# Performance work log

Measured on AMD Instinct MI355X. Metric: run time of the kernel, lower is better.

The kernel has to match this reference:

```python
import jax, jax.numpy as jnp
import numpy as np
from math import factorial as _fact

# ---- sizes / hyperparams (match init_kwargs) ----
N_NODES, N_EDGES = 8192, 131072
C, H, NRAD, NUM_LAYERS = 64, 64, 8, 2
R_MAX, AVG_NN = 5.0, 16.0
LS = (0, 1, 2)  # irreps degrees carried by node features and edge SH

# ---- real-basis Clebsch-Gordan coefficients (computed once in numpy) ----
def _cg_scalar(j1, m1, j2, m2, j3, m3):
    if m1 + m2 != m3:
        return 0.0
    pre = ((2*j3+1) * _fact(j1+j2-j3) * _fact(j1-j2+j3) * _fact(-j1+j2+j3)
           / _fact(j1+j2+j3+1)) ** 0.5
    pre *= (_fact(j1+m1)*_fact(j1-m1)*_fact(j2+m2)*_fact(j2-m2)
            * _fact(j3+m3)*_fact(j3-m3)) ** 0.5
    s = 0.0
    for k in range(max(0, j2-j3-m1, j1+m2-j3), min(j1+j2-j3, j1-m1, j2+m2)+1):
        s += (-1)**k / (_fact(k)*_fact(j1+j2-j3-k)*_fact(j1-m1-k)
                        * _fact(j2+m2-k)*_fact(j3-j2+m1+k)*_fact(j3-j1-m2+k))
    return pre * s

def _U_real(l):
    # unitary: Y_real = U @ Y_complex, components ordered m=-l..l
    U = np.zeros((2*l+1, 2*l+1), dtype=complex)
    s2 = 2 ** -0.5
    for m in range(-l, l+1):
        if m > 0:
            U[m+l, m+l] = (-1)**m * s2
            U[m+l, -m+l] = s2
        elif m == 0:
            U[l, l] = 1.0
        else:
            U[m+l, m+l] = 1j*s2
            U[m+l, -m+l] = -1j*(-1)**(-m)*s2
    return U

def _real_cg(l1, l2, l3):
    Cc = np.zeros((2*l1+1, 2*l2+1, 2*l3+1))
    for i1, m1 in enumerate(range(-l1, l1+1)):
        for i2, m2 in enumerate(range(-l2, l2+1)):
            m3 = m1 + m2
            if abs(m3) <= l3:
                Cc[i1, i2, m3+l3] = _cg_scalar(l1, m1, l2, m2, l3, m3)
    U1, U2, U3 = _U_real(l1), _U_real(l2), _U_real(l3)
    W = np.einsum('ia,jb,kc,abc->ijk', U1.conj(), U2.conj(), U3, Cc.astype(complex))
    W = W.real if np.linalg.norm(W.real) >= np.linalg.norm(W.imag) else W.imag
    W = W / np.linalg.norm(W) * (2*l3+1) ** 0.5  # component-style normalization
    return jnp.asarray(W, dtype=jnp.float32)

PATHS = [(l1, l2, l3) for l1 in LS for l2 in LS for l3 in LS
         if abs(l1 - l2) <= l3 <= l1 + l2]  # 15 tensor-product paths
CGS = [_real_cg(*p) for p in PATHS]
N_PATHS = len(PATHS)


def _sph(u):
    # real spherical harmonics of unit vectors, l=0,1,2, m=-l..l ordering
    x, y, z = u[:, 0], u[:, 1], u[:, 2]
    sh0 = jnp.ones((u.shape[0], 1), u.dtype)
    sh1 = jnp.sqrt(3.0) * jnp.stack([y, z, x], axis=-1)
    sh2 = jnp.stack([jnp.sqrt(15.0)*x*y, jnp.sqrt(15.0)*y*z,
                     jnp.sqrt(5.0)/2*(3*z*z - 1.0),
                     jnp.sqrt(15.0)*x*z, jnp.sqrt(15.0)/2*(x*x - y*y)], axis=-1)
    return (sh0, sh1, sh2)


def _forward(positions, embed, w_proj, mlp_w1, mlp_b1, mlp_w2, mlp_b2, mlp_w3,
             lin_self, gate_w, gate_b, species, senders, receivers):
    n = positions.shape[0]
    rel = (positions[receivers] - positions[senders]) / R_MAX  # [E,3]
    d = jnp.linalg.norm(rel, axis=-1)                          # [E]
    u = rel / jnp.maximum(d, 1e-6)[:, None]
    sh = _sph(u)
    freqs = jnp.arange(1, NRAD + 1, dtype=positions.dtype)
    xr = jnp.clip(d, 1e-4, 1.0)[:, None]
    basis = jnp.sqrt(2.0) * jnp.sin(freqs * jnp.pi * xr) / xr  # Bessel [E,NRAD]
    cut = 0.5 * (jnp.cos(jnp.pi * jnp.clip(d, 0.0, 1.0)) + 1.0)  # smooth cutoff

    # initial species embedding -> scalar (0e) features; l>0 start at zero
    x0 = embed[species] @ w_proj                                # [N,C]
    feats = [x0[:, :, None],
             jnp.zeros((n, C, 3), x0.dtype),
             jnp.zeros((n, C, 5), x0.dtype)]

    inv_sqrt_nn = 1.0 / jnp.sqrt(jnp.asarray(AVG_NN, x0.dtype))
    for i in range(NUM_LAYERS):
        # radial MLP -> per-path, per-channel edge weights
        h = jax.nn.silu(basis @ mlp_w1[i] + mlp_b1[i])
        h = jax.nn.silu(h @ mlp_w2[i] + mlp_b2[i])
        w = (h @ mlp_w3[i]).reshape(-1, N_PATHS, C) * cut[:, None, None]
        xg = [feats[l][senders] for l in LS]                    # edge gather
        msgs = [0.0, 0.0, 0.0]
        for p, (l1, l2, l3) in enumerate(PATHS):
            m = jnp.einsum('eci,ej,ijk->eck', xg[l1], sh[l2], CGS[p])
            msgs[l3] = msgs[l3] + m * w[:, p, :, None]
        agg = [jax.ops.segment_sum(msgs[l], receivers, num_segments=n) * inv_sqrt_nn
               for l in LS]
        # self-interaction linears + gated nonlinearity + skip
        y = [jnp.einsum('ncm,cd->ndm', agg[l], lin_self[i, l]) for l in LS]
        feats[0] = feats[0] + jax.nn.silu(y[0])
        g_in = feats[0][:, :, 0]                                # [N,C] scalars
        for l in (1, 2):
            g = jax.nn.sigmoid(g_in @ gate_w[i, l-1] + gate_b[i, l-1])
            feats[l] = feats[l] + g[:, :, None] * y[l]

    # alpha = 0.5 ** l per irrep, then flatten to [N, C*(1+3+5)]
    return jnp.concatenate([(feats[l] * (0.5 ** l)).reshape(n, -1) for l in LS],
                           axis=-1)


def setup_inputs() -> dict:
    key = jax.random.key(0)
    ks = jax.random.split(key, 12)
    f32 = jnp.float32
    return {
        'positions': jax.random.normal(ks[0], (N_NODES, 3), f32),
        'species': jax.random.randint(ks[1], (N_NODES,), 0, 5),
        'senders': jax.random.randint(ks[2], (N_EDGES,), 0, N_NODES),
        'receivers': jax.random.randint(ks[3], (N_EDGES,), 0, N_NODES),
        'embed': jax.random.normal(ks[4], (5, 32), f32),
        'w_proj': jax.random.normal(ks[5], (32, C), f32) / jnp.sqrt(32.0),
        'mlp_w1': jax.random.normal(ks[6], (NUM_LAYERS, NRAD, H), f32) / jnp.sqrt(float(NRAD)),
        'mlp_b1': jnp.zeros((NUM_LAYERS, H), f32),
        'mlp_w2': jax.random.normal(ks[7], (NUM_LAYERS, H, H), f32) / jnp.sqrt(float(H)),
        'mlp_b2': jnp.zeros((NUM_LAYERS, H), f32),
        'mlp_w3': jax.random.normal(ks[8], (NUM_LAYERS, H, N_PATHS * C), f32) / jnp.sqrt(float(H)),
        'lin_self': jax.random.normal(ks[9], (NUM_LAYERS, 3, C, C), f32) / jnp.sqrt(float(C)),
        'gate_w': jax.random.normal(ks[10], (NUM_LAYERS, 2, C, C), f32) / jnp.sqrt(float(C)),
        'gate_b': jnp.zeros((NUM_LAYERS, 2, C), f32),
    }


def reference(positions, species, senders, receivers, embed, w_proj, mlp_w1,
              mlp_b1, mlp_w2, mlp_b2, mlp_w3, lin_self, gate_w, gate_b):
    return _forward(positions, embed, w_proj, mlp_w1, mlp_b1, mlp_w2, mlp_b2,
                    mlp_w3, lin_self, gate_w, gate_b, species, senders, receivers)
```

## Files before the change

### kernel.cpp

```cpp
#include <hip/hip_runtime.h>
#include <cmath>
#include <algorithm>

#define N_NODES 8192
#define N_EDGES 131072
#define NPATHS 15
#define FPN 576
#define NODE_BLK 8
#define SWROW 968

typedef unsigned short ushortx;
typedef unsigned int uintx;
typedef short short8 __attribute__((ext_vector_type(8)));
typedef float f32x4 __attribute__((ext_vector_type(4)));

constexpr int PL1[NPATHS] = {0,0,0,1,1,1,1,1,1,2,2,2,2,2,2};
constexpr int PL2[NPATHS] = {0,1,2,0,1,1,1,2,2,0,1,1,2,2,2};
constexpr int PL3[NPATHS] = {0,1,2,1,0,1,2,1,2,2,1,2,0,1,2};
constexpr int CGOFF[NPATHS] = {0,1,10,35,44,53,80,125,170,245,270,315,390,415,490};
constexpr int CGTOT = 615;
constexpr int BOFF[3] = {0,1,4};

struct CGTable { float v[CGTOT]; };

constexpr double cfact(int n){ double r=1.0; for (int i=2;i<=n;++i) r*=i; return r; }
constexpr double csqrt(double x){
  if (x <= 0.0) return 0.0;
  double g = x < 1.0 ? 1.0 : x, p = 0.0;
  while (g != p){ p = g; g = 0.5*(g + x/g); }
  return g;
}
constexpr int cmax2(int a,int b){ return a>b?a:b; }
constexpr int cmin2(int a,int b){ return a<b?a:b; }

constexpr double cg_scalar_c(int j1,int m1,int j2,int m2,int j3,int m3){
  if (m1+m2 != m3) return 0.0;
  double pre = csqrt((2.0*j3+1.0)*cfact(j1+j2-j3)*cfact(j1-j2+j3)*cfact(-j1+j2+j3)/cfact(j1+j2+j3+1));
  pre *= csqrt(cfact(j1+m1)*cfact(j1-m1)*cfact(j2+m2)*cfact(j2-m2)*cfact(j3+m3)*cfact(j3-m3));
  double s = 0.0;
  int kmin = cmax2(0, cmax2(j2-j3-m1, j1+m2-j3));
  int kmax = cmin2(j1+j2-j3, cmin2(j1-m1, j2+m2));
  for (int k=kmin;k<=kmax;++k){
    double t = 1.0/(cfact(k)*cfact(j1+j2-j3-k)*cfact(j1-m1-k)*cfact(j2+m2-k)*cfact(j3-j2+m1+k)*cfact(j3-j1-m2+k));
    s += (k&1) ? -t : t;
  }
  return pre*s;
}

struct C2c { double re, im; };
constexpr C2c Uelem(int l, int a, int b){
  const double s2 = csqrt(0.5);
  const int m = a - l;
  C2c z{0.0, 0.0};
  if (m > 0){
    if (b ==  m+l) z = {((m&1)?-1.0:1.0)*s2, 0.0};
    else if (b == -m+l) z = {s2, 0.0};
  } else if (m == 0){
    if (b == l) z = {1.0, 0.0};
  } else {
    if (b ==  m+l) z = {0.0, s2};
    else if (b == -m+l) z = {0.0, -((((-m)&1))?-1.0:1.0)*s2};
  }
  return z;
}

constexpr CGTable build_cg(){
  CGTable t{};
  for (int p=0;p<NPATHS;++p){
    const int l1=PL1[p], l2=PL2[p], l3=PL3[p];
    const int n1=2*l1+1, n2=2*l2+1, n3=2*l3+1;
    double Cc[5][5][5] = {};
    for (int i1=0;i1<n1;++i1) for (int i2=0;i2<n2;++i2){
      int m1=i1-l1, m2=i2-l2, m3=m1+m2;
      if (m3 >= -l3 && m3 <= l3) Cc[i1][i2][m3+l3] = cg_scalar_c(l1,m1,l2,m2,l3,m3);
    }
    double Wre[5][5][5]={}, Wim[5][5][5]={};
    for (int i=0;i<n1;++i) for (int j=0;j<n2;++j) for (int k=0;k<n3;++k){
      double are=0.0, aim=0.0;
      for (int a=0;a<n1;++a) for (int b=0;b<n2;++b){
        int m3 = (a-l1)+(b-l2);
        if (m3 < -l3 || m3 > l3) continue;
        double cv = Cc[a][b][m3+l3];
        if (cv == 0.0) continue;
        C2c u1 = Uelem(l1,i,a);  u1.im = -u1.im;
        C2c u2 = Uelem(l2,j,b);  u2.im = -u2.im;
        C2c u3 = Uelem(l3,k,m3+l3);
        C2c u12{u1.re*u2.re - u1.im*u2.im, u1.re*u2.im + u1.im*u2.re};
        C2c tt {u12.re*u3.re - u12.im*u3.im, u12.re*u3.im + u12.im*u3.re};
        are += tt.re*cv; aim += tt.im*cv;
      }
      Wre[i][j][k]=are; Wim[i][j][k]=aim;
    }
    double nr=0.0, ni=0.0;
    for (int i=0;i<n1;++i) for (int j=0;j<n2;++j) for (int k=0;k<n3;++k){
      nr += Wre[i][j][k]*Wre[i][j][k]; ni += Wim[i][j][k]*Wim[i][j][k];
    }
    const bool useRe = csqrt(nr) >= csqrt(ni);
    const double nrm = csqrt(useRe ? nr : ni);
    const double scale = csqrt((double)n3) / nrm;
    for (int i=0;i<n1;++i) for (int j=0;j<n2;++j) for (int k=0;k<n3;++k)
      t.v[CGOFF[p] + (i*n2+j)*n3 + k] =
        (float)((useRe ? Wre[i][j][k] : Wim[i][j][k]) * scale);
  }
  return t;
}

inline constexpr CGTable CGC = build_cg();

__device__ __forceinline__ float siluf(float x){ return x / (1.0f + expf(-x)); }
__device__ __forceinline__ float sigmf(float x){ return 1.0f / (1.0f + expf(-x)); }
__device__ __forceinline__ ushortx f2b(float f){
  uintx u = __float_as_uint(f);
  u += 0x7fffu + ((u >> 16) & 1u);
  return (ushortx)(u >> 16);
}
__device__ __forceinline__ float b2f(ushortx b){ return __uint_as_float(((uintx)b) << 16); }

template<int L1, int L2, int P0, int NP>
__device__ __forceinline__ void tp_combo(const float* __restrict__ X,
                                         const float* __restrict__ S,
                                         const float* __restrict__ w,
                                         float* __restrict__ m)
{
  #pragma unroll
  for (int i=0;i<2*L1+1;++i){
    #pragma unroll
    for (int j=0;j<2*L2+1;++j){
      const float xs = X[BOFF[L1]+i] * S[BOFF[L2]+j];
      #pragma unroll
      for (int pp=0;pp<NP;++pp){
        const int p  = P0 + pp;
        const int l3 = PL3[p];
        const int n3 = 2*l3+1;
        const float t = w[p] * xs;
        #pragma unroll
        for (int k=0;k<n3;++k){
          const float c = CGC.v[CGOFF[p] + (i*(2*L2+1)+j)*n3 + k];
          if (c != 0.0f) m[BOFF[l3]+k] = fmaf(c, t, m[BOFF[l3]+k]);
        }
      }
    }
  }
}

__global__ __launch_bounds__(64) void k_init(const int* __restrict__ species,
    const float* __restrict__ embed, const float* __restrict__ wproj,
    float* __restrict__ feats)
{
  const int n = blockIdx.x, c = threadIdx.x;
  const int sp = species[n];
  float acc = 0.f;
  #pragma unroll
  for (int q=0;q<32;++q) acc += embed[sp*32+q]*wproj[q*64+c];
  feats[n*FPN + c] = acc;
  #pragma unroll
  for (int r=1;r<9;++r) feats[n*FPN + r*64 + c] = 0.f;
}

__global__ __launch_bounds__(64) void k_out_t(const float* __restrict__ feats,
                                              float* __restrict__ out)
{
  const int n = blockIdx.x, c = threadIdx.x;
  const float* f = feats + (size_t)n*FPN;
  float* o = out + (size_t)n*FPN;
  o[c] = f[c];
  #pragma unroll
  for (int mm=0;mm<3;++mm) o[64 + c*3 + mm] = f[(1+mm)*64 + c] * 0.5f;
  #pragma unroll
  for (int mm=0;mm<5;++mm) o[256 + c*5 + mm] = f[(4+mm)*64 + c] * 0.25f;
}

__global__ __launch_bounds__(256) void k_hist(const int* __restrict__ receivers,
                                              int* __restrict__ cnt)
{
  int e = blockIdx.x*256 + threadIdx.x;
  atomicAdd(&cnt[receivers[e]], 1);
}

__global__ __launch_bounds__(1024) void k_scan(const int* __restrict__ cnt,
    int* __restrict__ row_start, int* __restrict__ cursor)
{
  __shared__ int part[1024];
  const int t = threadIdx.x;
  int loc[8];
  #pragma unroll
  for (int i=0;i<8;++i) loc[i] = cnt[t*8+i];
  int sum = 0;
  #pragma unroll
  for (int i=0;i<8;++i) sum += loc[i];
  part[t] = sum;
  __syncthreads();
  for (int off=1; off<1024; off<<=1){
    int x = (t >= off) ? part[t-off] : 0;
    __syncthreads();
    part[t] += x;
    __syncthreads();
  }
  int run = (t > 0) ? part[t-1] : 0;
  #pragma unroll
  for (int i=0;i<8;++i){
    row_start[t*8+i] = run;
    cursor[t*8+i]    = run;
    run += loc[i];
  }
  if (t == 1023) row_start[8192] = run;
}

__global__ __launch_bounds__(256) void k_scatter(const int* __restrict__ receivers,
    int* __restrict__ cursor, int* __restrict__ perm)
{
  int e = blockIdx.x*256 + threadIdx.x;
  int r = receivers[e];
  int pos = atomicAdd(&cursor[r], 1);
  perm[pos] = e;
}

__global__ __launch_bounds__(256) void k_geom(const float* __restrict__ pos,
    const int* __restrict__ senders, const int* __restrict__ receivers,
    const int* __restrict__ perm,
    float* __restrict__ sh8s, float* __restrict__ d_s,
    int* __restrict__ send_s, int* __restrict__ recv_s)
{
  const int i = blockIdx.x*256 + threadIdx.x;
  const int e = perm[i];
  const int s = senders[e], r = receivers[e];
  send_s[i] = s;
  recv_s[i] = r;
  float rx = (pos[r*3+0] - pos[s*3+0]) * 0.2f;
  float ry = (pos[r*3+1] - pos[s*3+1]) * 0.2f;
  float rz = (pos[r*3+2] - pos[s*3+2]) * 0.2f;
  float d  = sqrtf(rx*rx + ry*ry + rz*rz);
  d_s[i] = d;
  float iv = 1.0f / fmaxf(d, 1e-6f);
  float x = rx*iv, y = ry*iv, z = rz*iv;
  const float s3   = 1.7320508075688772f;
  const float s15  = 3.8729833462074170f;
  const float s5h  = 1.1180339887498949f;
  const float s15h = 1.9364916731037085f;
  sh8s[i*8+0] = s3*y;
  sh8s[i*8+1] = s3*z;
  sh8s[i*8+2] = s3*x;
  sh8s[i*8+3] = s15*x*y;
  sh8s[i*8+4] = s15*y*z;
  sh8s[i*8+5] = s5h*(3.f*z*z - 1.f);
  sh8s[i*8+6] = s15*x*z;
  sh8s[i*8+7] = s15h*(x*x - y*y);
}

__global__ __launch_bounds__(256) void k_mlp(
    const float* __restrict__ d_s,
    const float* __restrict__ w1, const float* __restrict__ b1,
    const float* __restrict__ w2, const float* __restrict__ b2,
    ushortx* __restrict__ h2p)
{
  __shared__ float s_w2[4096];
  __shared__ float s_h1[4*64];
  const int tid = threadIdx.x, wv = tid>>6, lane = tid&63;
  const float PI = 3.14159265358979323846f;
  for (int i=tid;i<4096;i+=256) s_w2[i] = w2[i];
  __syncthreads();
  #pragma unroll
  for (int ee=0; ee<2; ++ee){
    const int i = blockIdx.x*8 + wv*2 + ee;
    const float d = d_s[i];
    float xr = fminf(fmaxf(d, 1e-4f), 1.0f);
    float ixr = 1.0f/xr;
    float acc = b1[lane];
    #pragma unroll
    for (int q=0;q<8;++q){
      float bs = 1.4142135623730951f * sinf((float)(q+1)*PI*xr) * ixr;
      acc = fmaf(bs, w1[q*64+lane], acc);
    }
    s_h1[wv*64+lane] = siluf(acc);
    __syncthreads();
    float acc2 = b2[lane];
    #pragma unroll
    for (int k=0;k<64;++k) acc2 = fmaf(s_h1[wv*64+k], s_w2[k*64+lane], acc2);
    float dc = fminf(fmaxf(d, 0.f), 1.f);
    float cut = 0.5f*(cosf(PI*dc) + 1.f);
    float h2 = siluf(acc2) * cut * 0.25f;
    h2p[(size_t)i*64+lane] = f2b(h2);
    __syncthreads();
  }
}

__global__ __launch_bounds__(256) void k_w3t(const float* __restrict__ w3,
                                             ushortx* __restrict__ w3t)
{
  int g = blockIdx.x*256 + threadIdx.x;
  int n = g >> 6, k = g & 63;
  w3t[g] = f2b(w3[k*960 + n]);
}

__global__ __launch_bounds__(256) void k_aggmm(
    const float* __restrict__ featsIn, float* __restrict__ featsOut,
    const ushortx* __restrict__ h2p, const ushortx* __restrict__ w3t,
    const float* __restrict__ sh8s, const int* __restrict__ send_s,
    const int* __restrict__ recv_s, const int* __restrict__ rowst,
    const float* __restrict__ lin, const float* __restrict__ gw,
    const float* __restrict__ gb)
{
  __shared__ float   s_agg[NODE_BLK*FPN];
  __shared__ ushortx s_w[16*SWROW];
  __shared__ ushortx s_a[16*72];

  const int tid  = threadIdx.x;
  const int wv   = tid >> 6;
  const int lane = tid & 63;
  const int n0   = blockIdx.x * NODE_BLK;
  const int beg  = rowst[n0];
  const int end  = rowst[n0 + NODE_BLK];

  for (int k = tid; k < NODE_BLK*FPN; k += 256) s_agg[k] = 0.f;
  __syncthreads();

  const int q = lane >> 4, mrow = lane & 15;

  for (int ebeg = beg; ebeg < end; ebeg += 16){
    {
      int er = tid >> 4, seg = tid & 15;
      int i = ebeg + er;
      if (i >= end) i = end - 1;
      *(uint2*)&s_a[er*72 + seg*4] =
        *(const uint2*)&h2p[(size_t)i*64 + seg*4];
    }
    __syncthreads();

    short8 a0 = *(const short8*)&s_a[mrow*72 +      q*8];
    short8 a1 = *(const short8*)&s_a[mrow*72 + 32 + q*8];
    #pragma unroll
    for (int nt=0; nt<15; ++nt){
      const int col = wv*240 + nt*16 + mrow;
      short8 b0 = *(const short8*)&w3t[(size_t)col*64 +      q*8];
      short8 b1 = *(const short8*)&w3t[(size_t)col*64 + 32 + q*8];
      f32x4 acc = {0.f,0.f,0.f,0.f};
      acc = __builtin_amdgcn_mfma_f32_16x16x32_bf16(a0, b0, acc, 0, 0, 0);
      acc = __builtin_amdgcn_mfma_f32_16x16x32_bf16(a1, b1, acc, 0, 0, 0);
      #pragma unroll
      for (int r=0;r<4;++r)
        s_w[(q*4+r)*SWROW + col] = f2b(acc[r]);
    }
    __syncthreads();

    #pragma unroll
    for (int ee=0; ee<4; ++ee){
      const int slot = wv*4 + ee;
      const int i = ebeg + slot;
      if (i < end){
        const int s  = send_s[i];
        const int rl = recv_s[i] - n0;
        const float* fb = featsIn + (size_t)s*FPN;
        float X[9];
        #pragma unroll
        for (int r=0;r<9;++r) X[r] = fb[r*64 + lane];
        float S[9];
        S[0] = 1.f;
        #pragma unroll
        for (int jj=0;jj<8;++jj) S[1+jj] = sh8s[(size_t)i*8+jj];
        float w[NPATHS];
        #pragma unroll
        for (int p=0;p<NPATHS;++p) w[p] = b2f(s_w[slot*SWROW + p*64 + lane]);
        float m[9];
        #pragma unroll
        for (int k=0;k<9;++k) m[k] = 0.f;

        tp_combo<0,0, 0,1>(X,S,w,m);
        tp_combo<0,1, 1,1>(X,S,w,m);
        tp_combo<0,2, 2,1>(X,S,w,m);
        tp_combo<1,0, 3,1>(X,S,w,m);
        tp_combo<1,1, 4,3>(X,S,w,m);
        tp_combo<1,2, 7,2>(X,S,w,m);
        tp_combo<2,0, 9,1>(X,S,w,m);
        tp_combo<2,1,10,2>(X,S,w,m);
        tp_combo<2,2,12,3>(X,S,w,m);

        float* ab = s_agg + rl*FPN;
        #pragma unroll
        for (int r=0;r<9;++r) atomicAdd(&ab[r*64 + lane], m[r]);
      }
    }
    __syncthreads();
  }

  #pragma unroll
  for (int k=0;k<2;++k){
    const int ln = wv*2 + k;
    const int n  = n0 + ln;
    const float* ag = s_agg + ln*FPN;
    float y[9];
    #pragma unroll
    for (int j=0;j<9;++j) y[j] = 0.f;
    for (int c=0;c<64;++c){
      float l0 = lin[          c*64 + lane];
      float l1 = lin[4096    + c*64 + lane];
      float l2 = lin[8192    + c*64 + lane];
      y[0] = fmaf(ag[c], l0, y[0]);
      #pragma unroll
      for (int mm=0;mm<3;++mm) y[1+mm] = fmaf(ag[(1+mm)*64 + c], l1, y[1+mm]);
      #pragma unroll
      for (int mm=0;mm<5;++mm) y[4+mm] = fmaf(ag[(4+mm)*64 + c], l2, y[4+mm]);
    }
    const size_t base = (size_t)n*FPN;
    float f0 = featsIn[base + lane] + siluf(y[0]);
    featsOut[base + lane] = f0;
    float a1 = gb[lane], a2 = gb[64 + lane];
    for (int c=0;c<64;++c){
      float fc = __shfl(f0, c);
      a1 = fmaf(fc, gw[        c*64 + lane], a1);
      a2 = fmaf(fc, gw[4096 +  c*64 + lane], a2);
    }
    float g1 = sigmf(a1), g2 = sigmf(a2);
    #pragma unroll
    for (int mm=0;mm<3;++mm)
      featsOut[base + (1+mm)*64 + lane] = featsIn[base + (1+mm)*64 + lane] + g1*y[1+mm];
    #pragma unroll
    for (int mm=0;mm<5;++mm)
      featsOut[base + (4+mm)*64 + lane] = featsIn[base + (4+mm)*64 + lane] + g2*y[4+mm];
  }
}

__global__ __launch_bounds__(64) void k_init_fb(const int* __restrict__ species,
    const float* __restrict__ embed, const float* __restrict__ wproj,
    float* __restrict__ feats)
{
  const int n = blockIdx.x, c = threadIdx.x;
  const int sp = species[n];
  float acc = 0.f;
  #pragma unroll
  for (int q=0;q<32;++q) acc += embed[sp*32+q]*wproj[q*64+c];
  feats[n*FPN + c] = acc;
  #pragma unroll
  for (int j=0;j<8;++j) feats[n*FPN + 64 + j*64 + c] = 0.f;
}

__global__ __launch_bounds__(256) void k_out_fb(const float* __restrict__ feats,
                                                float* __restrict__ out)
{
  const int n = blockIdx.x;
  for (int j = threadIdx.x; j < FPN; j += 256){
    float sc = (j < 64) ? 1.0f : ((j < 256) ? 0.5f : 0.25f);
    out[n*FPN + j] = feats[n*FPN + j] * sc;
  }
}

__global__ __launch_bounds__(256) void k_edge_fb(
    const float* __restrict__ pos,
    const int* __restrict__ senders, const int* __restrict__ receivers,
    const float* __restrict__ w1, const float* __restrict__ b1,
    const float* __restrict__ w2, const float* __restrict__ b2,
    const float* __restrict__ w3,
    const float* __restrict__ feats, float* __restrict__ agg,
    const CGTable cg)
{
  __shared__ float s_h1[16*64];
  __shared__ float s_h2[16*64];
  __shared__ float s_w3[8*960];
  __shared__ float s_sh[16][8];
  __shared__ float s_cut[16];

  const int tid  = threadIdx.x;
  const int wave = tid >> 6;
  const int lane = tid & 63;
  const int ebase = blockIdx.x * 16;
  const float PI = 3.14159265358979323846f;

  #pragma unroll
  for (int ee=0; ee<4; ++ee){
    const int slot = wave*4 + ee;
    const int e = ebase + slot;
    const int s = senders[e], r = receivers[e];
    float rx = (pos[r*3+0] - pos[s*3+0]) * 0.2f;
    float ry = (pos[r*3+1] - pos[s*3+1]) * 0.2f;
    float rz = (pos[r*3+2] - pos[s*3+2]) * 0.2f;
    float d  = sqrtf(rx*rx + ry*ry + rz*rz);
    float iv = 1.0f / fmaxf(d, 1e-6f);
    float x = rx*iv, y = ry*iv, z = rz*iv;
    if (lane == 0){
      const float s3   = 1.7320508075688772f;
      const float s15  = 3.8729833462074170f;
      const float s5h  = 1.1180339887498949f;
      const float s15h = 1.9364916731037085f;
      s_sh[slot][0] = s3*y;  s_sh[slot][1] = s3*z;  s_sh[slot][2] = s3*x;
      s_sh[slot][3] = s15*x*y; s_sh[slot][4] = s15*y*z;
      s_sh[slot][5] = s5h*(3.f*z*z - 1.f);
      s_sh[slot][6] = s15*x*z; s_sh[slot][7] = s15h*(x*x - y*y);
      float dc = fminf(fmaxf(d, 0.f), 1.f);
      s_cut[slot] = 0.5f*(cosf(PI*dc) + 1.f);
    }
    float xr = fminf(fmaxf(d, 1e-4f), 1.0f);
    float ixr = 1.0f/xr;
    float acc = b1[lane];
    #pragma unroll
    for (int q=0;q<8;++q)
      acc += 1.4142135623730951f * sinf((float)(q+1)*PI*xr) * ixr * w1[q*64 + lane];
    s_h1[slot*64 + lane] = siluf(acc);
  }
  __syncthreads();
  #pragma unroll
  for (int ee=0; ee<4; ++ee){
    const int slot = wave*4 + ee;
    float acc = b2[lane];
    #pragma unroll
    for (int k=0;k<64;++k) acc += s_h1[slot*64+k] * w2[k*64+lane];
    s_h2[slot*64+lane] = siluf(acc);
  }
  __syncthreads();

  float wgt[NPATHS][4];
  #pragma unroll
  for (int p=0;p<NPATHS;++p){ wgt[p][0]=wgt[p][1]=wgt[p][2]=wgt[p][3]=0.f; }
  for (int kc=0;kc<8;++kc){
    #pragma unroll
    for (int rr=0;rr<8;++rr){
      #pragma unroll
      for (int jj=0;jj<4;++jj){
        int col = jj*256 + tid;
        if (col < 960) s_w3[rr*960+col] = w3[(kc*8+rr)*960+col];
      }
    }
    __syncthreads();
    #pragma unroll
    for (int kk=0;kk<8;++kk){
      float h2v[4];
      #pragma unroll
      for (int ee=0;ee<4;++ee) h2v[ee] = s_h2[(wave*4+ee)*64 + kc*8+kk];
      #pragma unroll
      for (int p=0;p<NPATHS;++p){
        float wv = s_w3[kk*960 + p*64 + lane];
        #pragma unroll
        for (int ee=0;ee<4;++ee) wgt[p][ee] = fmaf(h2v[ee], wv, wgt[p][ee]);
      }
    }
    __syncthreads();
  }
  #pragma unroll
  for (int ee=0;ee<4;++ee){
    float f = s_cut[wave*4+ee] * 0.25f;
    #pragma unroll
    for (int p=0;p<NPATHS;++p) wgt[p][ee] *= f;
  }
  #pragma unroll
  for (int ee=0;ee<4;++ee){
    const int slot = wave*4 + ee;
    const int e = ebase + slot;
    const int s = senders[e];
    const int r = receivers[e];
    const int sb = s*FPN;
    float X[9], S[9], msg[9];
    X[0] = feats[sb + lane];
    #pragma unroll
    for (int mm=0;mm<3;++mm) X[1+mm] = feats[sb + 64  + lane*3 + mm];
    #pragma unroll
    for (int mm=0;mm<5;++mm) X[4+mm] = feats[sb + 256 + lane*5 + mm];
    S[0] = 1.f;
    #pragma unroll
    for (int j=0;j<8;++j) S[1+j] = s_sh[slot][j];
    #pragma unroll
    for (int k=0;k<9;++k) msg[k] = 0.f;
    #pragma unroll
    for (int p=0;p<NPATHS;++p){
      const int l1=PL1[p], l2=PL2[p], l3=PL3[p];
      const int n2=2*l2+1, n3=2*l3+1;
      const float wp = wgt[p][ee];
      #pragma unroll
      for (int i=0;i<2*l1+1;++i){
        #pragma unroll
        for (int j=0;j<n2;++j){
          float t = wp * X[BOFF[l1]+i] * S[BOFF[l2]+j];
          #pragma unroll
          for (int k=0;k<n3;++k)
            msg[BOFF[l3]+k] = fmaf(cg.v[CGOFF[p] + (i*n2+j)*n3 + k], t, msg[BOFF[l3]+k]);
        }
      }
    }
    const int rb = r*FPN;
    unsafeAtomicAdd(&agg[rb + lane], msg[0]);
    #pragma unroll
    for (int mm=0;mm<3;++mm) unsafeAtomicAdd(&agg[rb + 64  + lane*3 + mm], msg[1+mm]);
    #pragma unroll
    for (int mm=0;mm<5;++mm) unsafeAtomicAdd(&agg[rb + 256 + lane*5 + mm], msg[4+mm]);
  }
}

__global__ __launch_bounds__(64) void k_node_fb(
    float* __restrict__ feats, const float* __restrict__ agg,
    const float* __restrict__ lin, const float* __restrict__ gw,
    const float* __restrict__ gb)
{
  __shared__ float sf0[64];
  const int n = blockIdx.x, d = threadIdx.x;
  const int base = n*FPN;
  float y[9];
  #pragma unroll
  for (int k=0;k<9;++k) y[k]=0.f;
  for (int c=0;c<64;++c){
    float l0 = lin[          c*64 + d];
    float l1 = lin[4096    + c*64 + d];
    float l2 = lin[8192    + c*64 + d];
    y[0] = fmaf(agg[base + c], l0, y[0]);
    #pragma unroll
    for (int mm=0;mm<3;++mm) y[1+mm] = fmaf(agg[base + 64  + c*3 + mm], l1, y[1+mm]);
    #pragma unroll
    for (int mm=0;mm<5;++mm) y[4+mm] = fmaf(agg[base + 256 + c*5 + mm], l2, y[4+mm]);
  }
  float f0 = feats[base + d] + siluf(y[0]);
  feats[base + d] = f0;
  sf0[d] = f0;
  __syncthreads();
  {
    float acc = gb[d];
    for (int c=0;c<64;++c) acc = fmaf(sf0[c], gw[c*64 + d], acc);
    float g = sigmf(acc);
    #pragma unroll
    for (int mm=0;mm<3;++mm) feats[base + 64 + d*3 + mm] += g*y[1+mm];
  }
  {
    float acc = gb[64 + d];
    for (int c=0;c<64;++c) acc = fmaf(sf0[c], gw[4096 + c*64 + d], acc);
    float g = sigmf(acc);
    #pragma unroll
    for (int mm=0;mm<5;++mm) feats[base + 256 + d*5 + mm] += g*y[4+mm];
  }
}

extern "C" void kernel_launch(void* const* d_in, const int* in_sizes, int n_in,
                              void* d_out, int out_size, void* d_ws, size_t ws_size,
                              hipStream_t stream)
{
  const float* pos      = (const float*)d_in[0];
  const int*   species  = (const int*)  d_in[1];
  const int*   senders  = (const int*)  d_in[2];
  const int*   receivers= (const int*)  d_in[3];
  const float* embed    = (const float*)d_in[4];
  const float* wproj    = (const float*)d_in[5];
  const float* w1       = (const float*)d_in[6];
  const float* b1       = (const float*)d_in[7];
  const float* w2       = (const float*)d_in[8];
  const float* b2       = (const float*)d_in[9];
  const float* w3       = (const float*)d_in[10];
  const float* lin      = (const float*)d_in[11];
  const float* gw       = (const float*)d_in[12];
  const float* gb       = (const float*)d_in[13];

  char* p = (char*)d_ws;
  size_t off = 0;
  auto alloc = [&](size_t bytes)->char*{
    char* r = p + off;
    off += (bytes + 255) & ~(size_t)255;
    return r;
  };
  float*   featsA  = (float*)  alloc((size_t)N_NODES*FPN*4);
  float*   featsB  = (float*)  alloc((size_t)N_NODES*FPN*4);
  int*     cnt     = (int*)    alloc(N_NODES*4);
  int*     cursor  = (int*)    alloc(N_NODES*4);
  int*     rowst   = (int*)    alloc((N_NODES+1)*4);
  int*     perm    = (int*)    alloc((size_t)N_EDGES*4);
  int*     send_s  = (int*)    alloc((size_t)N_EDGES*4);
  int*     recv_s  = (int*)    alloc((size_t)N_EDGES*4);
  float*   d_sArr  = (float*)  alloc((size_t)N_EDGES*4);
  float*   sh8s    = (float*)  alloc((size_t)N_EDGES*8*4);
  ushortx* h2p     = (ushortx*)alloc((size_t)N_EDGES*64*2);
  ushortx* w3t     = (ushortx*)alloc((size_t)960*64*2);
  const size_t need_main = off;

  if (ws_size >= need_main){
    hipMemsetAsync(cnt, 0, N_NODES*4, stream);
    hipLaunchKernelGGL(k_hist,    dim3(N_EDGES/256), dim3(256), 0, stream, receivers, cnt);
    hipLaunchKernelGGL(k_scan,    dim3(1), dim3(1024), 0, stream, cnt, rowst, cursor);
    hipLaunchKernelGGL(k_scatter, dim3(N_EDGES/256), dim3(256), 0, stream, receivers, cursor, perm);
    hipLaunchKernelGGL(k_geom,    dim3(N_EDGES/256), dim3(256), 0, stream,
                       pos, senders, receivers, perm, sh8s, d_sArr, send_s, recv_s);
    hipLaunchKernelGGL(k_init,    dim3(N_NODES), dim3(64), 0, stream,
                       species, embed, wproj, featsA);
    for (int L=0; L<2; ++L){
      const float* fin  = (L == 0) ? featsA : featsB;
      float*       fout = (L == 0) ? featsB : featsA;
      hipLaunchKernelGGL(k_mlp,  dim3(N_EDGES/8), dim3(256), 0, stream,
                         d_sArr, w1 + L*512, b1 + L*64, w2 + L*4096, b2 + L*64, h2p);
      hipLaunchKernelGGL(k_w3t,  dim3(240), dim3(256), 0, stream, w3 + (size_t)L*61440, w3t);
      hipLaunchKernelGGL(k_aggmm, dim3(N_NODES/NODE_BLK), dim3(256), 0, stream,
                         fin, fout, h2p, w3t, sh8s, send_s, recv_s, rowst,
                         lin + L*3*64*64, gw + L*2*64*64, gb + L*2*64);
    }
    hipLaunchKernelGGL(k_out_t, dim3(N_NODES), dim3(64), 0, stream, featsA, (float*)d_out);
  } else {
    float* feats = (float*)d_ws;
    float* agg   = feats + (size_t)N_NODES*FPN;
    hipLaunchKernelGGL(k_init_fb, dim3(N_NODES), dim3(64), 0, stream,
                       species, embed, wproj, feats);
    for (int L=0; L<2; ++L){
      hipMemsetAsync(agg, 0, (size_t)N_NODES*FPN*sizeof(float), stream);
      hipLaunchKernelGGL(k_edge_fb, dim3(N_EDGES/16), dim3(256), 0, stream,
                         pos, senders, receivers,
                         w1 + L*512, b1 + L*64, w2 + L*4096, b2 + L*64,
                         w3 + (size_t)L*61440, feats, agg, CGC);
      hipLaunchKernelGGL(k_node_fb, dim3(N_NODES), dim3(64), 0, stream,
                         feats, agg, lin + L*3*64*64, gw + L*2*64*64, gb + L*2*64);
    }
    hipLaunchKernelGGL(k_out_fb, dim3(N_NODES), dim3(256), 0, stream, feats, (float*)d_out);
  }
}
```

Baseline: 1.409 ms.

## Give each wave its own edges and drop block-wide barriers in edge loop

Each wave now processes its own group of 4 edges. It computes the full 960-column edge-weight MFMA for those edges straight from global h2p, and writes the results to its own rows of shared memory. This removes the shared staging buffer for the edge features and the two __syncthreads per 16-edge step, so waves no longer wait on each other. In exchange, every wave computes all 60 column tiles with only 4 of the 16 MFMA rows being unique. That means about four times more MFMA work and w3t loads per edge.

```diff
diff --git a/kernel.cpp b/kernel.cpp
--- a/kernel.cpp
+++ b/kernel.cpp
@@ -302,7 +302,6 @@
 {
   __shared__ float   s_agg[NODE_BLK*FPN];
   __shared__ ushortx s_w[16*SWROW];
-  __shared__ ushortx s_a[16*72];
 
   const int tid  = threadIdx.x;
   const int wv   = tid >> 6;
@@ -316,36 +315,30 @@
 
   const int q = lane >> 4, mrow = lane & 15;
 
-  for (int ebeg = beg; ebeg < end; ebeg += 16){
-    {
-      int er = tid >> 4, seg = tid & 15;
-      int i = ebeg + er;
-      if (i >= end) i = end - 1;
-      *(uint2*)&s_a[er*72 + seg*4] =
-        *(const uint2*)&h2p[(size_t)i*64 + seg*4];
-    }
-    __syncthreads();
-
-    short8 a0 = *(const short8*)&s_a[mrow*72 +      q*8];
-    short8 a1 = *(const short8*)&s_a[mrow*72 + 32 + q*8];
-    #pragma unroll
-    for (int nt=0; nt<15; ++nt){
-      const int col = wv*240 + nt*16 + mrow;
+  for (int i0 = beg + wv*4; i0 < end; i0 += 16){
+    int ia = i0 + (mrow & 3);
+    if (ia >= end) ia = end - 1;
+    short8 a0 = *(const short8*)&h2p[(size_t)ia*64 +      q*8];
+    short8 a1 = *(const short8*)&h2p[(size_t)ia*64 + 32 + q*8];
+
+    #pragma unroll 4
+    for (int t=0; t<60; ++t){
+      const int col = t*16 + mrow;
       short8 b0 = *(const short8*)&w3t[(size_t)col*64 +      q*8];
       short8 b1 = *(const short8*)&w3t[(size_t)col*64 + 32 + q*8];
       f32x4 acc = {0.f,0.f,0.f,0.f};
       acc = __builtin_amdgcn_mfma_f32_16x16x32_bf16(a0, b0, acc, 0, 0, 0);
       acc = __builtin_amdgcn_mfma_f32_16x16x32_bf16(a1, b1, acc, 0, 0, 0);
-      #pragma unroll
-      for (int r=0;r<4;++r)
-        s_w[(q*4+r)*SWROW + col] = f2b(acc[r]);
-    }
-    __syncthreads();
+      if (q == 0){
+        #pragma unroll
+        for (int r=0;r<4;++r)
+          s_w[(wv*4+r)*SWROW + col] = f2b(acc[r]);
+      }
+    }
 
     #pragma unroll
     for (int ee=0; ee<4; ++ee){
-      const int slot = wv*4 + ee;
-      const int i = ebeg + slot;
+      const int i = i0 + ee;
       if (i < end){
         const int s  = send_s[i];
         const int rl = recv_s[i] - n0;
@@ -359,7 +352,7 @@
         for (int jj=0;jj<8;++jj) S[1+jj] = sh8s[(size_t)i*8+jj];
         float w[NPATHS];
         #pragma unroll
-        for (int p=0;p<NPATHS;++p) w[p] = b2f(s_w[slot*SWROW + p*64 + lane]);
+        for (int p=0;p<NPATHS;++p) w[p] = b2f(s_w[(wv*4+ee)*SWROW + p*64 + lane]);
         float m[9];
         #pragma unroll
         for (int k=0;k<9;++k) m[k] = 0.f;
@@ -379,8 +372,8 @@
         for (int r=0;r<9;++r) atomicAdd(&ab[r*64 + lane], m[r]);
       }
     }
-    __syncthreads();
-  }
+  }
+  __syncthreads();
 
   #pragma unroll
   for (int k=0;k<2;++k){
```

After: 2.447 ms. 73.7% more time.

## Split fused aggregate-matmul into separate MFMA weight GEMM and aggregation kernels

Applied to the files above, without the earlier changes.

Replaces the fused k_aggmm kernel with two kernels when workspace allows. k_gemmW computes per-edge path weights with bf16 MFMA into a materialized bf16 buffer laid out channel-major per edge, and k_aggS reads those weights for the tensor product, scatter-add and node update. This removes the per-block shared-memory weight staging and GEMM from the aggregation loop. In exchange it adds a large intermediate (about 256 MB when unchunked) written and read through global memory, plus node-range chunking that adds launches when workspace is small.

```diff
diff --git a/kernel.cpp b/kernel.cpp
--- a/kernel.cpp
+++ b/kernel.cpp
@@ -115,6 +115,8 @@
   return (ushortx)(u >> 16);
 }
 __device__ __forceinline__ float b2f(ushortx b){ return __uint_as_float(((uintx)b) << 16); }
+__device__ __forceinline__ float blo(uintx u){ return __uint_as_float(u << 16); }
+__device__ __forceinline__ float bhi(uintx u){ return __uint_as_float(u & 0xffff0000u); }
 
 template<int L1, int L2, int P0, int NP>
 __device__ __forceinline__ void tp_combo(const float* __restrict__ X,
@@ -292,6 +294,138 @@
   w3t[g] = f2b(w3[k*960 + n]);
 }
 
+__global__ __launch_bounds__(256) void k_gemmW(
+    const ushortx* __restrict__ h2p, const ushortx* __restrict__ w3t,
+    const int* __restrict__ rowst, int n0c, int n1c,
+    ushortx* __restrict__ wgt, int capE)
+{
+  const int eBeg = rowst[n0c], eEnd = rowst[n1c];
+  const int e0 = eBeg + blockIdx.x*16;
+  if (e0 >= eEnd) return;
+  const int tid = threadIdx.x, wv = tid >> 6, lane = tid & 63;
+  const int q = lane >> 4, mrow = lane & 15;
+
+  int ia = e0 + mrow;
+  if (ia >= eEnd) ia = eEnd - 1;
+  short8 a0 = *(const short8*)&h2p[(size_t)ia*64 +      q*8];
+  short8 a1 = *(const short8*)&h2p[(size_t)ia*64 + 32 + q*8];
+
+  #pragma unroll
+  for (int nt=0; nt<15; ++nt){
+    const int col = wv*240 + nt*16 + mrow;
+    short8 b0 = *(const short8*)&w3t[(size_t)col*64 +      q*8];
+    short8 b1 = *(const short8*)&w3t[(size_t)col*64 + 32 + q*8];
+    f32x4 acc = {0.f,0.f,0.f,0.f};
+    acc = __builtin_amdgcn_mfma_f32_16x16x32_bf16(a0, b0, acc, 0, 0, 0);
+    acc = __builtin_amdgcn_mfma_f32_16x16x32_bf16(a1, b1, acc, 0, 0, 0);
+    const int p = col >> 6, ch = col & 63;
+    #pragma unroll
+    for (int r=0;r<4;++r){
+      const int erow = e0 + q*4 + r;
+      const int rel  = erow - eBeg;
+      if (erow < eEnd && rel < capE)
+        wgt[(size_t)rel*1024 + ch*16 + p] = f2b(acc[r]);
+    }
+  }
+}
+
+__global__ __launch_bounds__(256) void k_aggS(
+    const float* __restrict__ featsIn, float* __restrict__ featsOut,
+    const ushortx* __restrict__ wgt, const float* __restrict__ sh8s,
+    const int* __restrict__ send_s, const int* __restrict__ recv_s,
+    const int* __restrict__ rowst, int n0c,
+    const float* __restrict__ lin, const float* __restrict__ gw,
+    const float* __restrict__ gb, int capE)
+{
+  __shared__ float s_agg[NODE_BLK*FPN];
+
+  const int tid  = threadIdx.x;
+  const int wv   = tid >> 6;
+  const int lane = tid & 63;
+  const int n0   = n0c + blockIdx.x * NODE_BLK;
+  const int beg  = rowst[n0];
+  const int end  = rowst[n0 + NODE_BLK];
+  const int eBeg = rowst[n0c];
+
+  for (int k = tid; k < NODE_BLK*FPN; k += 256) s_agg[k] = 0.f;
+  __syncthreads();
+
+  for (int i = beg + wv; i < end; i += 4){
+    const int s  = send_s[i];
+    const int rl = recv_s[i] - n0;
+    const float* fb = featsIn + (size_t)s*FPN;
+    float X[9];
+    #pragma unroll
+    for (int r=0;r<9;++r) X[r] = fb[r*64 + lane];
+    float S[9];
+    S[0] = 1.f;
+    #pragma unroll
+    for (int jj=0;jj<8;++jj) S[1+jj] = sh8s[(size_t)i*8+jj];
+    const int rel = i - eBeg;
+    const uint4* wp = (const uint4*)(wgt + (size_t)(rel < capE ? rel : capE-1)*1024 + lane*16);
+    uint4 ua = wp[0], ub = wp[1];
+    float w[NPATHS];
+    w[0]=blo(ua.x);  w[1]=bhi(ua.x);  w[2]=blo(ua.y);  w[3]=bhi(ua.y);
+    w[4]=blo(ua.z);  w[5]=bhi(ua.z);  w[6]=blo(ua.w);  w[7]=bhi(ua.w);
+    w[8]=blo(ub.x);  w[9]=bhi(ub.x);  w[10]=blo(ub.y); w[11]=bhi(ub.y);
+    w[12]=blo(ub.z); w[13]=bhi(ub.z); w[14]=blo(ub.w);
+    float m[9];
+    #pragma unroll
+    for (int k=0;k<9;++k) m[k] = 0.f;
+
+    tp_combo<0,0, 0,1>(X,S,w,m);
+    tp_combo<0,1, 1,1>(X,S,w,m);
+    tp_combo<0,2, 2,1>(X,S,w,m);
+    tp_combo<1,0, 3,1>(X,S,w,m);
+    tp_combo<1,1, 4,3>(X,S,w,m);
+    tp_combo<1,2, 7,2>(X,S,w,m);
+    tp_combo<2,0, 9,1>(X,S,w,m);
+    tp_combo<2,1,10,2>(X,S,w,m);
+    tp_combo<2,2,12,3>(X,S,w,m);
+
+    float* ab = s_agg + rl*FPN;
+    #pragma unroll
+    for (int r=0;r<9;++r) atomicAdd(&ab[r*64 + lane], m[r]);
+  }
+  __syncthreads();
+
+  #pragma unroll
+  for (int k=0;k<2;++k){
+    const int ln = wv*2 + k;
+    const int n  = n0 + ln;
+    const float* ag = s_agg + ln*FPN;
+    float y[9];
+    #pragma unroll
+    for (int j=0;j<9;++j) y[j] = 0.f;
+    for (int c=0;c<64;++c){
+      float l0 = lin[          c*64 + lane];
+      float l1 = lin[4096    + c*64 + lane];
+      float l2 = lin[8192    + c*64 + lane];
+      y[0] = fmaf(ag[c], l0, y[0]);
+      #pragma unroll
+      for (int mm=0;mm<3;++mm) y[1+mm] = fmaf(ag[(1+mm)*64 + c], l1, y[1+mm]);
+      #pragma unroll
+      for (int mm=0;mm<5;++mm) y[4+mm] = fmaf(ag[(4+mm)*64 + c], l2, y[4+mm]);
+    }
+    const size_t base = (size_t)n*FPN;
+    float f0 = featsIn[base + lane] + siluf(y[0]);
+    featsOut[base + lane] = f0;
+    float a1 = gb[lane], a2 = gb[64 + lane];
+    for (int c=0;c<64;++c){
+      float fc = __shfl(f0, c);
+      a1 = fmaf(fc, gw[        c*64 + lane], a1);
+      a2 = fmaf(fc, gw[4096 +  c*64 + lane], a2);
+    }
+    float g1 = sigmf(a1), g2 = sigmf(a2);
+    #pragma unroll
+    for (int mm=0;mm<3;++mm)
+      featsOut[base + (1+mm)*64 + lane] = featsIn[base + (1+mm)*64 + lane] + g1*y[1+mm];
+    #pragma unroll
+    for (int mm=0;mm<5;++mm)
+      featsOut[base + (4+mm)*64 + lane] = featsIn[base + (4+mm)*64 + lane] + g2*y[4+mm];
+  }
+}
+
 __global__ __launch_bounds__(256) void k_aggmm(
     const float* __restrict__ featsIn, float* __restrict__ featsOut,
     const ushortx* __restrict__ h2p, const ushortx* __restrict__ w3t,
@@ -661,9 +795,17 @@
   float*   sh8s    = (float*)  alloc((size_t)N_EDGES*8*4);
   ushortx* h2p     = (ushortx*)alloc((size_t)N_EDGES*64*2);
   ushortx* w3t     = (ushortx*)alloc((size_t)960*64*2);
-  const size_t need_main = off;
-
-  if (ws_size >= need_main){
+  const size_t need_common = off;
+
+  int strideN = 0;
+  size_t capE = 0;
+  const int strides[4] = {8192, 4096, 2048, 1024};
+  for (int t=0; t<4; ++t){
+    size_t cap = (size_t)strides[t]*16 + ((strides[t] == 8192) ? 0 : 2048);
+    if (need_common + cap*2048 <= ws_size){ strideN = strides[t]; capE = cap; break; }
+  }
+
+  if (need_common <= ws_size){
     hipMemsetAsync(cnt, 0, N_NODES*4, stream);
     hipLaunchKernelGGL(k_hist,    dim3(N_EDGES/256), dim3(256), 0, stream, receivers, cnt);
     hipLaunchKernelGGL(k_scan,    dim3(1), dim3(1024), 0, stream, cnt, rowst, cursor);
@@ -672,15 +814,35 @@
                        pos, senders, receivers, perm, sh8s, d_sArr, send_s, recv_s);
     hipLaunchKernelGGL(k_init,    dim3(N_NODES), dim3(64), 0, stream,
                        species, embed, wproj, featsA);
-    for (int L=0; L<2; ++L){
-      const float* fin  = (L == 0) ? featsA : featsB;
-      float*       fout = (L == 0) ? featsB : featsA;
-      hipLaunchKernelGGL(k_mlp,  dim3(N_EDGES/8), dim3(256), 0, stream,
-                         d_sArr, w1 + L*512, b1 + L*64, w2 + L*4096, b2 + L*64, h2p);
-      hipLaunchKernelGGL(k_w3t,  dim3(240), dim3(256), 0, stream, w3 + (size_t)L*61440, w3t);
-      hipLaunchKernelGGL(k_aggmm, dim3(N_NODES/NODE_BLK), dim3(256), 0, stream,
-                         fin, fout, h2p, w3t, sh8s, send_s, recv_s, rowst,
-                         lin + L*3*64*64, gw + L*2*64*64, gb + L*2*64);
+    if (strideN > 0){
+      ushortx* wgt = (ushortx*)alloc(capE*2048);
+      const int chunks = N_NODES / strideN;
+      for (int L=0; L<2; ++L){
+        const float* fin  = (L == 0) ? featsA : featsB;
+        float*       fout = (L == 0) ? featsB : featsA;
+        hipLaunchKernelGGL(k_mlp,  dim3(N_EDGES/8), dim3(256), 0, stream,
+                           d_sArr, w1 + L*512, b1 + L*64, w2 + L*4096, b2 + L*64, h2p);
+        hipLaunchKernelGGL(k_w3t,  dim3(240), dim3(256), 0, stream, w3 + (size_t)L*61440, w3t);
+        for (int c=0; c<chunks; ++c){
+          const int n0c = c*strideN, n1c = n0c + strideN;
+          hipLaunchKernelGGL(k_gemmW, dim3((unsigned)(capE/16)), dim3(256), 0, stream,
+                             h2p, w3t, rowst, n0c, n1c, wgt, (int)capE);
+          hipLaunchKernelGGL(k_aggS, dim3(strideN/NODE_BLK), dim3(256), 0, stream,
+                             fin, fout, wgt, sh8s, send_s, recv_s, rowst, n0c,
+                             lin + L*3*64*64, gw + L*2*64*64, gb + L*2*64, (int)capE);
+        }
+      }
+    } else {
+      for (int L=0; L<2; ++L){
+        const float* fin  = (L == 0) ? featsA : featsB;
+        float*       fout = (L == 0) ? featsB : featsA;
+        hipLaunchKernelGGL(k_mlp,  dim3(N_EDGES/8), dim3(256), 0, stream,
+                           d_sArr, w1 + L*512, b1 + L*64, w2 + L*4096, b2 + L*64, h2p);
+        hipLaunchKernelGGL(k_w3t,  dim3(240), dim3(256), 0, stream, w3 + (size_t)L*61440, w3t);
+        hipLaunchKernelGGL(k_aggmm, dim3(N_NODES/NODE_BLK), dim3(256), 0, stream,
+                           fin, fout, h2p, w3t, sh8s, send_s, recv_s, rowst,
+                           lin + L*3*64*64, gw + L*2*64*64, gb + L*2*64);
+      }
     }
     hipLaunchKernelGGL(k_out_t, dim3(N_NODES), dim3(64), 0, stream, featsA, (float*)d_out);
   } else {
```

Result: slower. 2.078 ms (+47.4%).
